# Optimization experiments

Hardware: AMD Instinct MI355X
Metric: run time of the kernel (lower is better)

The kernel has to match this reference:

```python
import jax, jax.numpy as jnp
import numpy as np

B, S, C, H, W = 4, 32, 128, 32, 32
HID = 128


def setup_inputs() -> dict:
    key = jax.random.key(0)
    ks = jax.random.split(key, 8)
    s_conv = 1.0 / np.sqrt((C + HID) * 9)
    s_fc = 1.0 / np.sqrt(HID)
    s_head = 1.0 / np.sqrt(C)
    return {
        "x": jax.random.normal(ks[0], (B, S, C, H, W), jnp.float32),
        "conv_w": jax.random.normal(ks[1], (4 * HID, C + HID, 3, 3), jnp.float32) * s_conv,
        "conv_b": jnp.zeros((4 * HID,), jnp.float32),
        "init_h": jax.random.normal(ks[2], (HID,), jnp.float32) * 0.01,
        "init_c": jax.random.normal(ks[3], (HID,), jnp.float32) * 0.01,
        "fc_w": jax.random.normal(ks[4], (C, HID), jnp.float32) * s_fc,
        "fc_b": jnp.zeros((C,), jnp.float32),
        "fco_w": jax.random.normal(ks[5], (1, C), jnp.float32) * s_head,
        "fco_b": jnp.zeros((1,), jnp.float32),
        "fca_w": jax.random.normal(ks[6], (1, C), jnp.float32) * s_head,
        "fca_b": jnp.zeros((1,), jnp.float32),
    }


def reference(x, conv_w, conv_b, init_h, init_c, fc_w, fc_b, fco_w, fco_b, fca_w, fca_b):
    b, s, c, h_, w_ = x.shape
    hid = init_h.shape[0]
    # broadcast learned init state over batch + spatial dims
    h0 = jnp.broadcast_to(init_h[None, :, None, None], (b, hid, h_, w_))
    c0 = jnp.broadcast_to(init_c[None, :, None, None], (b, hid, h_, w_))

    def step(carry, xt):
        h, cst = carry
        z = jnp.concatenate([xt, h], axis=1)  # [B, C+hid, H, W]
        gates = jax.lax.conv_general_dilated(
            z, conv_w, (1, 1), 'SAME',
            dimension_numbers=('NCHW', 'OIHW', 'NCHW')
        ) + conv_b[None, :, None, None]
        i, f, o, g = jnp.split(gates, 4, axis=1)
        i = jax.nn.sigmoid(i)
        f = jax.nn.sigmoid(f)
        o = jax.nn.sigmoid(o)
        g = jnp.tanh(g)  # activation='tanh' (relu_lstm=False)
        c_next = f * cst + i * g
        h_next = o * jnp.tanh(c_next)
        return (h_next, c_next), h_next  # skip=False -> y_step == h_next

    _, ys = jax.lax.scan(step, (h0, c0), jnp.swapaxes(x, 0, 1))  # ys: [S,B,hid,H,W]
    y = jnp.swapaxes(ys, 0, 1)  # [B,S,hid,H,W]
    feat = y.mean(axis=(3, 4))  # AdaptiveAvgPool2d((1,1)) -> [B,S,hid]
    feat = jax.nn.relu(feat @ fc_w.T + fc_b)  # [B,S,C]
    offset = feat @ fco_w.T + fco_b  # [B,S,1]
    angle = feat @ fca_w.T + fca_b   # [B,S,1]
    return (offset, angle)
```

## Files before the change

kernel.cpp:

```cpp
#include <hip/hip_runtime.h>
#include <math.h>

#define BB 4
#define SS 32
#define CCH 128
#define PLANE 1024
#define ZP 34
#define NOC 512
#define NIC 256

#define LDSA 18432
#define LDSZ 21760
#define LDSB (LDSA + LDSZ)

typedef _Float16 f16;
typedef _Float16 f16x8 __attribute__((ext_vector_type(8)));
typedef float f32x4 __attribute__((ext_vector_type(4)));

__device__ __forceinline__ float sigmoidf_(float v) { return 1.0f / (1.0f + __expf(-v)); }

__device__ __forceinline__ void gload16(const void* g, void* l) {
    __builtin_amdgcn_global_load_lds(
        (const __attribute__((address_space(1))) void*)g,
        (__attribute__((address_space(3))) void*)l, 16, 0, 0);
}

__global__ void wprep_kernel(const float* __restrict__ w, f16* __restrict__ wt) {
    int idx = blockIdx.x * 256 + threadIdx.x;
    if (idx >= 9 * 512 * 256) return;
    int ic  = idx & 255;
    int ocp = (idx >> 8) & 511;
    int tap = idx >> 17;
    int hc = ocp >> 2, g = ocp & 3;
    int oc = g * 128 + hc;
    wt[idx] = (f16)w[((size_t)(oc * 256 + ic)) * 9 + tap];
}

__global__ __launch_bounds__(256) void init_kernel(
    const float* __restrict__ x, const float* __restrict__ ih,
    const float* __restrict__ icst, f16* __restrict__ zpad0,
    f16* __restrict__ zpad1, float* __restrict__ cst, float* __restrict__ feat)
{
    int bx = blockIdx.x;
    int b = bx / 34, y = bx % 34;
    int ch = threadIdx.x;
    f16* z0row = zpad0 + (((size_t)b * ZP + y) * ZP) * NIC;
    f16* z1row = zpad1 + (((size_t)b * ZP + y) * ZP) * NIC;
    bool border_y = (y == 0) | (y == 33);
    for (int xx = 0; xx < 34; ++xx) {
        bool border = border_y || xx == 0 || xx == 33;
        float v;
        if (border) v = 0.f;
        else if (ch < 128) v = x[((((size_t)b * SS + 0) * CCH + ch) * 32 + (y - 1)) * 32 + (xx - 1)];
        else v = ih[ch - 128];
        z0row[xx * NIC + ch] = (f16)v;
        if (border) z1row[xx * NIC + ch] = (f16)0.f;
    }
    if (y >= 1 && y <= 32 && ch < 128) {
        float cv = icst[ch];
        float* cr = cst + ((size_t)b * 128 + ch) * PLANE + (y - 1) * 32;
        for (int xx = 0; xx < 32; ++xx) cr[xx] = cv;
    }
    if (y == 33) {
        for (int k = 0; k < 16; ++k) feat[(size_t)b * 4096 + ch + k * 256] = 0.f;
    }
}

__global__ __launch_bounds__(256) void step_kernel(
    const f16* __restrict__ wt, const f16* __restrict__ zread,
    f16* __restrict__ zwrite, const float* __restrict__ x,
    const float* __restrict__ bias, float* __restrict__ cst,
    float* __restrict__ feat, int t)
{
    __shared__ unsigned char LDS[2 * LDSB];
    __shared__ float redbuf[4][8];

    const int bid = blockIdx.x;
    const int mt = bid & 15;
    const int nt = (bid >> 4) & 3;
    const int b  = bid >> 6;
    const int tid = threadIdx.x;
    const int lane = tid & 63;
    const int wc = tid >> 6;

    const f16* srcb[10];
    int soff[10];
    #pragma unroll
    for (int r = 0; r < 10; ++r) {
        int s = tid + r * 256;
        if (s < 1152) {
            int tap = s >> 7, rem = s & 127;
            int p = rem >> 2, q = rem & 3;
            int qs = q ^ ((p >> 1) & 3);
            srcb[r] = wt + ((size_t)(tap * NOC + mt * 32 + p)) * NIC + qs * 8;
        } else {
            int z = s - 1152;
            int p = z >> 2; if (p > 339) p = 339;
            int q = z & 3;
            int qs = q ^ ((p >> 1) & 3);
            int row = p / 34, xx = p - row * 34;
            srcb[r] = zread + (((size_t)b * ZP + nt * 8 + row) * ZP + xx) * NIC + qs * 8;
        }
        soff[r] = s * 16;
    }

    f32x4 acc[2][4];
    #pragma unroll
    for (int i = 0; i < 2; ++i)
        #pragma unroll
        for (int j = 0; j < 4; ++j) acc[i][j] = (f32x4){0.f, 0.f, 0.f, 0.f};

    auto stage = [&](int bufsel, int icc) {
        int ico = icc * 32;
        #pragma unroll
        for (int r = 0; r < 10; ++r) {
            if (r < 9 || tid < 208)
                gload16(srcb[r] + ico, LDS + bufsel * LDSB + soff[r]);
        }
    };

    auto compute = [&](int bufsel) {
        const unsigned char* Ab = LDS + bufsel * LDSB;
        const unsigned char* Zb = Ab + LDSA;
        const int q = lane >> 4;
        #pragma unroll
        for (int tap = 0; tap < 9; ++tap) {
            const int dy = tap / 3, dx = tap - dy * 3;
            f16x8 af[2], bf[4];
            #pragma unroll
            for (int fm = 0; fm < 2; ++fm) {
                int p = fm * 16 + (lane & 15);
                af[fm] = *(const f16x8*)(Ab + (tap * 128 + p * 4 + (q ^ ((p >> 1) & 3))) * 16);
            }
            #pragma unroll
            for (int fn = 0; fn < 4; ++fn) {
                int n = wc * 64 + fn * 16 + (lane & 15);
                int p = ((n >> 5) + dy) * 34 + (n & 31) + dx;
                bf[fn] = *(const f16x8*)(Zb + (p * 4 + (q ^ ((p >> 1) & 3))) * 16);
            }
            #pragma unroll
            for (int fm = 0; fm < 2; ++fm)
                #pragma unroll
                for (int fn = 0; fn < 4; ++fn)
                    acc[fm][fn] = __builtin_amdgcn_mfma_f32_16x16x32_f16(
                        af[fm], bf[fn], acc[fm][fn], 0, 0, 0);
        }
    };

    stage(0, 0);
    #pragma unroll
    for (int icc = 0; icc < 8; ++icc) {
        if (icc < 7) stage((icc + 1) & 1, icc + 1);
        if (icc < 7) asm volatile("s_waitcnt vmcnt(10)" ::: "memory");
        else         asm volatile("s_waitcnt vmcnt(0)" ::: "memory");
        __builtin_amdgcn_s_barrier();
        asm volatile("" ::: "memory");
        compute(icc & 1);
        asm volatile("" ::: "memory");
        __builtin_amdgcn_s_barrier();
    }

    const int q4 = lane >> 4;
    const int pxl = lane & 15;
    float psum[2];
    #pragma unroll
    for (int fm = 0; fm < 2; ++fm) {
        const int hc = mt * 8 + fm * 4 + q4;
        const float bi = bias[hc], bff = bias[128 + hc];
        const float bo = bias[256 + hc], bg = bias[384 + hc];
        psum[fm] = 0.f;
        #pragma unroll
        for (int fn = 0; fn < 4; ++fn) {
            int px = nt * 256 + wc * 64 + fn * 16 + pxl;
            f32x4 a = acc[fm][fn];
            float iv = sigmoidf_(a.x + bi);
            float fv = sigmoidf_(a.y + bff);
            float ov = sigmoidf_(a.z + bo);
            float gv = tanhf(a.w + bg);
            size_t co = ((size_t)b * 128 + hc) * PLANE + px;
            float cp = cst[co];
            float cn = fv * cp + iv * gv;
            float hn = ov * tanhf(cn);
            cst[co] = cn;
            int row = px >> 5, col = px & 31;
            zwrite[(((size_t)b * ZP + row + 1) * ZP + col + 1) * NIC + 128 + hc] = (f16)hn;
            psum[fm] += hn;
        }
    }
    #pragma unroll
    for (int m = 1; m < 16; m <<= 1) {
        psum[0] += __shfl_xor(psum[0], m, 64);
        psum[1] += __shfl_xor(psum[1], m, 64);
    }
    if (pxl == 0) {
        redbuf[wc][q4]     = psum[0];
        redbuf[wc][4 + q4] = psum[1];
    }

    if (t + 1 < SS) {
        int ch = mt * 8 + (tid >> 5);
        int pos = (tid & 31) * 8;
        int row = pos >> 5, col = pos & 31;
        const float* xs = x + (((size_t)b * SS + t + 1) * CCH + ch) * PLANE + nt * 256 + pos;
        f16* zd = zwrite + (((size_t)b * ZP + nt * 8 + row + 1) * ZP + col + 1) * NIC + ch;
        #pragma unroll
        for (int k = 0; k < 8; ++k) zd[k * NIC] = (f16)xs[k];
    }

    __syncthreads();
    if (tid < 8) {
        float s = redbuf[0][tid] + redbuf[1][tid] + redbuf[2][tid] + redbuf[3][tid];
        int fm = tid >> 2;
        int hc = mt * 8 + fm * 4 + (tid & 3);
        hc = mt * 8 + tid;
        atomicAdd(feat + ((size_t)b * SS + t) * 128 + hc, s * (1.f / 1024.f));
    }
}

__global__ __launch_bounds__(128) void head_kernel(
    const float* __restrict__ feat, const float* __restrict__ fcw,
    const float* __restrict__ fcb, const float* __restrict__ fcow,
    const float* __restrict__ fcob, const float* __restrict__ fcaw,
    const float* __restrict__ fcab, float* __restrict__ out)
{
    __shared__ float sf[128];
    __shared__ float redo[2], reda[2];
    int bs = blockIdx.x;
    int c  = threadIdx.x;
    sf[c] = feat[(size_t)bs * 128 + c];
    __syncthreads();
    float a = fcb[c];
    #pragma unroll 8
    for (int k = 0; k < 128; ++k) a = fmaf(fcw[c * 128 + k], sf[k], a);
    a = fmaxf(a, 0.0f);
    float po = a * fcow[c], pa = a * fcaw[c];
    #pragma unroll
    for (int off = 32; off > 0; off >>= 1) {
        po += __shfl_down(po, off, 64);
        pa += __shfl_down(pa, off, 64);
    }
    if ((c & 63) == 0) { redo[c >> 6] = po; reda[c >> 6] = pa; }
    __syncthreads();
    if (c == 0) {
        out[bs]       = redo[0] + redo[1] + fcob[0];
        out[128 + bs] = reda[0] + reda[1] + fcab[0];
    }
}

extern "C" void kernel_launch(void* const* d_in, const int* in_sizes, int n_in,
                              void* d_out, int out_size, void* d_ws, size_t ws_size,
                              hipStream_t stream) {
    const float* x      = (const float*)d_in[0];
    const float* conv_w = (const float*)d_in[1];
    const float* conv_b = (const float*)d_in[2];
    const float* init_h = (const float*)d_in[3];
    const float* init_c = (const float*)d_in[4];
    const float* fc_w   = (const float*)d_in[5];
    const float* fc_b   = (const float*)d_in[6];
    const float* fco_w  = (const float*)d_in[7];
    const float* fco_b  = (const float*)d_in[8];
    const float* fca_w  = (const float*)d_in[9];
    const float* fca_b  = (const float*)d_in[10];

    unsigned char* wsb = (unsigned char*)d_ws;
    size_t off = 0;
    f16* wt = (f16*)(wsb + off);       off += (size_t)9 * 512 * 256 * 2;
    off = (off + 255) & ~(size_t)255;
    f16* zpad0 = (f16*)(wsb + off);    off += (size_t)BB * ZP * ZP * NIC * 2;
    off = (off + 255) & ~(size_t)255;
    f16* zpad1 = (f16*)(wsb + off);    off += (size_t)BB * ZP * ZP * NIC * 2;
    off = (off + 255) & ~(size_t)255;
    float* cst = (float*)(wsb + off);  off += (size_t)BB * 128 * PLANE * 4;
    off = (off + 255) & ~(size_t)255;
    float* feat = (float*)(wsb + off); off += (size_t)BB * SS * 128 * 4;

    wprep_kernel<<<(9 * 512 * 256 + 255) / 256, 256, 0, stream>>>(conv_w, wt);
    init_kernel<<<BB * 34, 256, 0, stream>>>(x, init_h, init_c, zpad0, zpad1, cst, feat);

    f16* zb[2] = { zpad0, zpad1 };
    for (int t = 0; t < SS; ++t) {
        step_kernel<<<256, 256, 0, stream>>>(
            wt, zb[t & 1], zb[(t + 1) & 1], x, conv_b, cst, feat, t);
    }

    head_kernel<<<BB * SS, 128, 0, stream>>>(
        feat, fc_w, fc_b, fco_w, fco_b, fca_w, fca_b, (float*)d_out);
}
```

Before: 767.7 us.

## Transpose h and x writes through LDS, prefetch MFMA fragments, use fast tanh

```diff
diff --git a/kernel.cpp b/kernel.cpp
--- a/kernel.cpp
+++ b/kernel.cpp
@@ -18,6 +18,7 @@
 typedef float f32x4 __attribute__((ext_vector_type(4)));
 
 __device__ __forceinline__ float sigmoidf_(float v) { return 1.0f / (1.0f + __expf(-v)); }
+__device__ __forceinline__ float tanhf_(float v) { return 2.0f / (1.0f + __expf(-2.0f * v)) - 1.0f; }
 
 __device__ __forceinline__ void gload16(const void* g, void* l) {
     __builtin_amdgcn_global_load_lds(
@@ -74,6 +75,7 @@
 {
     __shared__ unsigned char LDS[2 * LDSB];
     __shared__ float redbuf[4][8];
+    __shared__ f16 tbuf[256][8];
 
     const int bid = blockIdx.x;
     const int mt = bid & 15;
@@ -119,31 +121,43 @@
         }
     };
 
+    const int q = lane >> 4;
+    const int l15 = lane & 15;
+
     auto compute = [&](int bufsel) {
         const unsigned char* Ab = LDS + bufsel * LDSB;
         const unsigned char* Zb = Ab + LDSA;
-        const int q = lane >> 4;
+        auto ldA = [&](int tap, int fm) -> f16x8 {
+            int p = fm * 16 + l15;
+            return *(const f16x8*)(Ab + (tap * 128 + p * 4 + (q ^ ((p >> 1) & 3))) * 16);
+        };
+        auto ldB = [&](int tap, int fn) -> f16x8 {
+            int dy = tap / 3, dx = tap - dy * 3;
+            int n = wc * 64 + fn * 16 + l15;
+            int p = ((n >> 5) + dy) * 34 + (n & 31) + dx;
+            return *(const f16x8*)(Zb + (p * 4 + (q ^ ((p >> 1) & 3))) * 16);
+        };
+        f16x8 a0 = ldA(0, 0), a1 = ldA(0, 1);
+        f16x8 b0 = ldB(0, 0), b1 = ldB(0, 1), b2 = ldB(0, 2), b3 = ldB(0, 3);
         #pragma unroll
         for (int tap = 0; tap < 9; ++tap) {
-            const int dy = tap / 3, dx = tap - dy * 3;
-            f16x8 af[2], bf[4];
-            #pragma unroll
-            for (int fm = 0; fm < 2; ++fm) {
-                int p = fm * 16 + (lane & 15);
-                af[fm] = *(const f16x8*)(Ab + (tap * 128 + p * 4 + (q ^ ((p >> 1) & 3))) * 16);
+            f16x8 na0, na1, nb0, nb1, nb2, nb3;
+            if (tap < 8) {
+                na0 = ldA(tap + 1, 0); na1 = ldA(tap + 1, 1);
+                nb0 = ldB(tap + 1, 0); nb1 = ldB(tap + 1, 1);
+                nb2 = ldB(tap + 1, 2); nb3 = ldB(tap + 1, 3);
+            } else {
+                na0 = a0; na1 = a1; nb0 = b0; nb1 = b1; nb2 = b2; nb3 = b3;
             }
-            #pragma unroll
-            for (int fn = 0; fn < 4; ++fn) {
-                int n = wc * 64 + fn * 16 + (lane & 15);
-                int p = ((n >> 5) + dy) * 34 + (n & 31) + dx;
-                bf[fn] = *(const f16x8*)(Zb + (p * 4 + (q ^ ((p >> 1) & 3))) * 16);
-            }
-            #pragma unroll
-            for (int fm = 0; fm < 2; ++fm)
-                #pragma unroll
-                for (int fn = 0; fn < 4; ++fn)
-                    acc[fm][fn] = __builtin_amdgcn_mfma_f32_16x16x32_f16(
-                        af[fm], bf[fn], acc[fm][fn], 0, 0, 0);
+            acc[0][0] = __builtin_amdgcn_mfma_f32_16x16x32_f16(a0, b0, acc[0][0], 0, 0, 0);
+            acc[1][0] = __builtin_amdgcn_mfma_f32_16x16x32_f16(a1, b0, acc[1][0], 0, 0, 0);
+            acc[0][1] = __builtin_amdgcn_mfma_f32_16x16x32_f16(a0, b1, acc[0][1], 0, 0, 0);
+            acc[1][1] = __builtin_amdgcn_mfma_f32_16x16x32_f16(a1, b1, acc[1][1], 0, 0, 0);
+            acc[0][2] = __builtin_amdgcn_mfma_f32_16x16x32_f16(a0, b2, acc[0][2], 0, 0, 0);
+            acc[1][2] = __builtin_amdgcn_mfma_f32_16x16x32_f16(a1, b2, acc[1][2], 0, 0, 0);
+            acc[0][3] = __builtin_amdgcn_mfma_f32_16x16x32_f16(a0, b3, acc[0][3], 0, 0, 0);
+            acc[1][3] = __builtin_amdgcn_mfma_f32_16x16x32_f16(a1, b3, acc[1][3], 0, 0, 0);
+            a0 = na0; a1 = na1; b0 = nb0; b1 = nb1; b2 = nb2; b3 = nb3;
         }
     };
 
@@ -160,30 +174,28 @@
         __builtin_amdgcn_s_barrier();
     }
 
-    const int q4 = lane >> 4;
-    const int pxl = lane & 15;
     float psum[2];
     #pragma unroll
     for (int fm = 0; fm < 2; ++fm) {
-        const int hc = mt * 8 + fm * 4 + q4;
+        const int hcl = fm * 4 + q;
+        const int hc = mt * 8 + hcl;
         const float bi = bias[hc], bff = bias[128 + hc];
         const float bo = bias[256 + hc], bg = bias[384 + hc];
         psum[fm] = 0.f;
         #pragma unroll
         for (int fn = 0; fn < 4; ++fn) {
-            int px = nt * 256 + wc * 64 + fn * 16 + pxl;
+            int pxloc = wc * 64 + fn * 16 + l15;
             f32x4 a = acc[fm][fn];
             float iv = sigmoidf_(a.x + bi);
             float fv = sigmoidf_(a.y + bff);
             float ov = sigmoidf_(a.z + bo);
-            float gv = tanhf(a.w + bg);
-            size_t co = ((size_t)b * 128 + hc) * PLANE + px;
+            float gv = tanhf_(a.w + bg);
+            size_t co = ((size_t)b * 128 + hc) * PLANE + nt * 256 + pxloc;
             float cp = cst[co];
             float cn = fv * cp + iv * gv;
-            float hn = ov * tanhf(cn);
+            float hn = ov * tanhf_(cn);
             cst[co] = cn;
-            int row = px >> 5, col = px & 31;
-            zwrite[(((size_t)b * ZP + row + 1) * ZP + col + 1) * NIC + 128 + hc] = (f16)hn;
+            tbuf[pxloc][hcl] = (f16)hn;
             psum[fm] += hn;
         }
     }
@@ -192,28 +204,40 @@
         psum[0] += __shfl_xor(psum[0], m, 64);
         psum[1] += __shfl_xor(psum[1], m, 64);
     }
-    if (pxl == 0) {
-        redbuf[wc][q4]     = psum[0];
-        redbuf[wc][4 + q4] = psum[1];
-    }
-
-    if (t + 1 < SS) {
-        int ch = mt * 8 + (tid >> 5);
-        int pos = (tid & 31) * 8;
-        int row = pos >> 5, col = pos & 31;
-        const float* xs = x + (((size_t)b * SS + t + 1) * CCH + ch) * PLANE + nt * 256 + pos;
-        f16* zd = zwrite + (((size_t)b * ZP + nt * 8 + row + 1) * ZP + col + 1) * NIC + ch;
-        #pragma unroll
-        for (int k = 0; k < 8; ++k) zd[k * NIC] = (f16)xs[k];
-    }
-
+    if (l15 == 0) {
+        redbuf[wc][q]     = psum[0];
+        redbuf[wc][4 + q] = psum[1];
+    }
     __syncthreads();
+
+    {
+        f16x8 v = *(const f16x8*)tbuf[tid];
+        int row = tid >> 5, col = tid & 31;
+        *(f16x8*)(zwrite + (((size_t)b * ZP + nt * 8 + row + 1) * ZP + col + 1) * NIC
+                  + 128 + mt * 8) = v;
+    }
     if (tid < 8) {
         float s = redbuf[0][tid] + redbuf[1][tid] + redbuf[2][tid] + redbuf[3][tid];
-        int fm = tid >> 2;
-        int hc = mt * 8 + fm * 4 + (tid & 3);
-        hc = mt * 8 + tid;
-        atomicAdd(feat + ((size_t)b * SS + t) * 128 + hc, s * (1.f / 1024.f));
+        atomicAdd(feat + ((size_t)b * SS + t) * 128 + mt * 8 + tid, s * (1.f / 1024.f));
+    }
+
+    if (t + 1 < SS) {
+        __syncthreads();
+        int ch = tid >> 5;
+        int pos = (tid & 31) * 8;
+        const float* xs = x + (((size_t)b * SS + t + 1) * CCH + mt * 8 + ch) * PLANE
+                          + nt * 256 + pos;
+        float4 v0 = *(const float4*)xs;
+        float4 v1 = *(const float4*)(xs + 4);
+        tbuf[pos + 0][ch] = (f16)v0.x; tbuf[pos + 1][ch] = (f16)v0.y;
+        tbuf[pos + 2][ch] = (f16)v0.z; tbuf[pos + 3][ch] = (f16)v0.w;
+        tbuf[pos + 4][ch] = (f16)v1.x; tbuf[pos + 5][ch] = (f16)v1.y;
+        tbuf[pos + 6][ch] = (f16)v1.z; tbuf[pos + 7][ch] = (f16)v1.w;
+        __syncthreads();
+        f16x8 v = *(const f16x8*)tbuf[tid];
+        int row = tid >> 5, col = tid & 31;
+        *(f16x8*)(zwrite + (((size_t)b * ZP + nt * 8 + row + 1) * ZP + col + 1) * NIC
+                  + mt * 8) = v;
     }
 }
 
```

Measured after the change: 729.1 us. 5.0% less time.
